# Kernel optimization log

Hardware: AMD Instinct MI355X
Metric: run time of the kernel (lower is better)

## Reference

```python
import jax, jax.numpy as jnp
import numpy as np

N_NODES = 100000
N_EDGES = 3200000
N_GRAPHS = 256
D = 3
H = 32


def _pointnet_layer(h, pos, src, dst, Wa, ba, Wb, bb):
    # PyG convention: edge_index = [src(j), dst(i)]; message uses h_j, pos_j - pos_i
    edge_feat = jnp.concatenate([h[src], pos[src] - pos[dst]], axis=-1)  # [E, Cin+D]
    msg = jax.nn.relu(edge_feat @ Wa + ba) @ Wb + bb                     # [E, H]
    agg = jax.ops.segment_max(msg, dst, num_segments=N_NODES)           # [N, H]
    # PyG scatter-max fills nodes with no incoming edges with 0
    return jnp.where(jnp.isneginf(agg), 0.0, agg)


def setup_inputs() -> dict:
    key = jax.random.key(0)
    ks = jax.random.split(key, 12)
    pos = jax.random.normal(ks[0], (N_NODES, D), dtype=jnp.float32)
    edge_index = jax.random.randint(ks[1], (2, N_EDGES), 0, N_NODES, dtype=jnp.int32)
    batch = jnp.sort(jax.random.randint(ks[2], (N_NODES,), 0, N_GRAPHS, dtype=jnp.int32))
    def lin(k, fan_in, fan_out):
        bound = 1.0 / np.sqrt(fan_in)
        kw, kb = jax.random.split(k)
        W = jax.random.uniform(kw, (fan_in, fan_out), minval=-bound, maxval=bound, dtype=jnp.float32)
        b = jax.random.uniform(kb, (fan_out,), minval=-bound, maxval=bound, dtype=jnp.float32)
        return W, b
    W1a, b1a = lin(ks[3], D + D, H)
    W1b, b1b = lin(ks[4], H, H)
    W2a, b2a = lin(ks[5], H + D, H)
    W2b, b2b = lin(ks[6], H, H)
    Wout, bout = lin(ks[7], H, 1)
    return {"pos": pos, "edge_index": edge_index, "batch": batch,
            "W1a": W1a, "b1a": b1a, "W1b": W1b, "b1b": b1b,
            "W2a": W2a, "b2a": b2a, "W2b": W2b, "b2b": b2b,
            "Wout": Wout, "bout": bout}


def reference(pos, edge_index, batch, W1a, b1a, W1b, b1b, W2a, b2a, W2b, b2b, Wout, bout):
    src, dst = edge_index[0], edge_index[1]
    h = _pointnet_layer(pos, pos, src, dst, W1a, b1a, W1b, b1b)
    h = jax.nn.relu(h)
    h = _pointnet_layer(h, pos, src, dst, W2a, b2a, W2b, b2b)
    h = jax.nn.relu(h)
    g = jax.ops.segment_max(h, batch, num_segments=N_GRAPHS)  # global_max_pool -> [B, H]
    g = jnp.where(jnp.isneginf(g), 0.0, g)
    return g @ Wout + bout  # [B, 1]
```

## Files before the change

### kernel.cpp

```cpp
#include <hip/hip_runtime.h>

#define NN 100000
#define NE 3200000
#define NG 256
#define H 32
#define SB ((NN + 255) / 256)
#define NB 98
#define BK_SH 10
#define PART_BLOCKS ((NE + 4095) / 4096)

typedef __attribute__((ext_vector_type(8))) short b16x8;
typedef __attribute__((ext_vector_type(4))) float f32x4;

union ABfrag { unsigned u[4]; b16x8 v; };

__global__ __launch_bounds__(256) void k_init(unsigned* __restrict__ g,
                                              unsigned* __restrict__ hist,
                                              unsigned* __restrict__ bktcnt) {
    int i = blockIdx.x * 256 + threadIdx.x;
    if (i < NG * H) g[i] = 0u;
    if (i < NN) hist[i] = 0u;
    if (i < NB) bktcnt[i] = 0u;
}

__global__ __launch_bounds__(64) void k_packw(const float* __restrict__ W1b,
                                              const float* __restrict__ W2b,
                                              unsigned* __restrict__ Wpk) {
    int l = threadIdx.x;
    int n = l & 15, gq = l >> 4;
    for (int layer = 0; layer < 2; layer++) {
        const float* W = layer ? W2b : W1b;
        for (int h = 0; h < 2; h++) {
            unsigned hi[8], lo[8];
#pragma unroll
            for (int i = 0; i < 8; i++) {
                float w = W[(8 * gq + i) * H + h * 16 + n];
                unsigned wb = __float_as_uint(w);
                unsigned hb = wb & 0xffff0000u;
                float r = w - __uint_as_float(hb);
                hi[i] = hb;
                lo[i] = __float_as_uint(r) & 0xffff0000u;
            }
            unsigned* dh = Wpk + (((layer * 4 + h * 2 + 0) * 64) + l) * 4;
            unsigned* dl = Wpk + (((layer * 4 + h * 2 + 1) * 64) + l) * 4;
#pragma unroll
            for (int w2 = 0; w2 < 4; w2++) {
                dh[w2] = (hi[2 * w2] >> 16) | (hi[2 * w2 + 1] & 0xffff0000u);
                dl[w2] = (lo[2 * w2] >> 16) | (lo[2 * w2 + 1] & 0xffff0000u);
            }
        }
    }
}

__global__ __launch_bounds__(256) void k_hist(const int* __restrict__ dst,
                                              unsigned* __restrict__ hist,
                                              unsigned* __restrict__ bktcnt) {
    __shared__ unsigned lb[NB];
    int tid = threadIdx.x;
    if (tid < NB) lb[tid] = 0u;
    __syncthreads();
    int base = blockIdx.x * 4096 + tid;
    for (int c = 0; c < 16; c++) {
        int e = base + c * 256;
        if (e < NE) {
            int d = dst[e];
            atomicAdd(&hist[d], 1u);
            atomicAdd(&lb[d >> BK_SH], 1u);
        }
    }
    __syncthreads();
    if (tid < NB) {
        unsigned v = lb[tid];
        if (v) atomicAdd(&bktcnt[tid], v);
    }
}

__global__ __launch_bounds__(256) void k_scan1(const unsigned* __restrict__ hist,
                                               unsigned* __restrict__ pre,
                                               unsigned* __restrict__ bsum) {
    __shared__ unsigned sd[256];
    int tid = threadIdx.x;
    int i = blockIdx.x * 256 + tid;
    unsigned v = (i < NN) ? hist[i] : 0u;
    sd[tid] = v;
    __syncthreads();
    for (int off = 1; off < 256; off <<= 1) {
        unsigned t = (tid >= off) ? sd[tid - off] : 0u;
        __syncthreads();
        sd[tid] += t;
        __syncthreads();
    }
    if (i < NN) pre[i] = sd[tid] - v;
    if (tid == 255) bsum[blockIdx.x] = sd[255];
}

__global__ __launch_bounds__(512) void k_scan2(const unsigned* __restrict__ bsum,
                                               unsigned* __restrict__ bpre) {
    __shared__ unsigned sd[512];
    int t = threadIdx.x;
    unsigned v = (t < SB) ? bsum[t] : 0u;
    sd[t] = v;
    __syncthreads();
    for (int off = 1; off < 512; off <<= 1) {
        unsigned x = (t >= off) ? sd[t - off] : 0u;
        __syncthreads();
        sd[t] += x;
        __syncthreads();
    }
    if (t < SB) bpre[t] = sd[t] - v;
}

__global__ __launch_bounds__(256) void k_scan3(const unsigned* __restrict__ pre,
                                               const unsigned* __restrict__ bpre,
                                               const unsigned* __restrict__ hist,
                                               unsigned* __restrict__ cursors,
                                               unsigned* __restrict__ ends) {
    int i = blockIdx.x * 256 + threadIdx.x;
    if (i < NN) {
        unsigned o = pre[i] + bpre[blockIdx.x];
        cursors[i] = o;
        ends[i] = o + hist[i];
    }
}

__global__ __launch_bounds__(128) void k_bscan(const unsigned* __restrict__ bktcnt,
                                               unsigned* __restrict__ bktbase,
                                               unsigned* __restrict__ bktcur) {
    __shared__ unsigned sd[128];
    int t = threadIdx.x;
    unsigned v = (t < NB) ? bktcnt[t] : 0u;
    sd[t] = v;
    __syncthreads();
    for (int off = 1; off < 128; off <<= 1) {
        unsigned x = (t >= off) ? sd[t - off] : 0u;
        __syncthreads();
        sd[t] += x;
        __syncthreads();
    }
    if (t < NB) { bktbase[t] = sd[t] - v; bktcur[t] = sd[t] - v; }
    if (t == 127) bktbase[NB] = NE;
}

__global__ __launch_bounds__(256) void k_part(const int* __restrict__ src,
                                              const int* __restrict__ dst,
                                              unsigned* __restrict__ bktcur,
                                              unsigned* __restrict__ staging) {
    __shared__ unsigned lh[NB], lcur[NB];
    int tid = threadIdx.x;
    if (tid < NB) lh[tid] = 0u;
    __syncthreads();
    int base = blockIdx.x * 4096 + tid;
    for (int c = 0; c < 16; c++) {
        int e = base + c * 256;
        if (e < NE) atomicAdd(&lh[dst[e] >> BK_SH], 1u);
    }
    __syncthreads();
    if (tid < NB) {
        unsigned v = lh[tid];
        lcur[tid] = v ? atomicAdd(&bktcur[tid], v) : 0u;
    }
    __syncthreads();
    for (int c = 0; c < 16; c++) {
        int e = base + c * 256;
        if (e < NE) {
            int d = dst[e], s = src[e];
            unsigned off = atomicAdd(&lcur[d >> BK_SH], 1u);
            staging[off] = ((unsigned)s << BK_SH) | (unsigned)(d & ((1 << BK_SH) - 1));
        }
    }
}

__global__ __launch_bounds__(256) void k_scat2(const unsigned* __restrict__ staging,
                                               const unsigned* __restrict__ bktbase,
                                               unsigned* __restrict__ cursors,
                                               unsigned* __restrict__ srcS) {
    int i = blockIdx.x * 256 + threadIdx.x;
    unsigned p = staging[i];
    int lo = 0, hi = NB - 1;
    while (lo < hi) {
        int mid = (lo + hi + 1) >> 1;
        if ((unsigned)i >= bktbase[mid]) lo = mid; else hi = mid - 1;
    }
    int d = (lo << BK_SH) | (int)(p & ((1u << BK_SH) - 1));
    unsigned slot = atomicAdd(&cursors[d], 1u);
    srcS[slot] = p >> BK_SH;
}

__global__ __launch_bounds__(256) void k_pre1(const float* __restrict__ pos,
                                              const float* __restrict__ W1a,
                                              const float* __restrict__ b1a,
                                              float* __restrict__ E) {
    int n = blockIdx.x * 256 + threadIdx.x;
    if (n >= NN) return;
    float p0 = pos[3 * n], p1 = pos[3 * n + 1], p2 = pos[3 * n + 2];
    float ev[H];
#pragma unroll
    for (int k = 0; k < H; k++) {
        float v = b1a[k];
        v = fmaf(p0, W1a[k] + W1a[96 + k], v);
        v = fmaf(p1, W1a[32 + k] + W1a[128 + k], v);
        v = fmaf(p2, W1a[64 + k] + W1a[160 + k], v);
        ev[k] = v;
    }
    float4* E4 = (float4*)(E + (size_t)n * H);
#pragma unroll
    for (int r = 0; r < 8; r++)
        E4[r] = make_float4(ev[4 * r], ev[4 * r + 1], ev[4 * r + 2], ev[4 * r + 3]);
}

__global__ __launch_bounds__(256) void k_pre2(const float* __restrict__ pos,
                                              const float* __restrict__ agg,
                                              const float* __restrict__ W2a,
                                              const float* __restrict__ b2a,
                                              float* __restrict__ E) {
    int n = blockIdx.x * 256 + threadIdx.x;
    if (n >= NN) return;
    float h[H];
    const float4* A4 = (const float4*)(agg + (size_t)n * H);
#pragma unroll
    for (int r = 0; r < 8; r++) {
        float4 u = A4[r];
        h[4 * r + 0] = u.x; h[4 * r + 1] = u.y;
        h[4 * r + 2] = u.z; h[4 * r + 3] = u.w;
    }
    float p0 = pos[3 * n], p1 = pos[3 * n + 1], p2 = pos[3 * n + 2];
    float ev[H];
#pragma unroll
    for (int k = 0; k < H; k++) {
        float v = b2a[k];
        v = fmaf(p0, W2a[32 * H + k], v);
        v = fmaf(p1, W2a[33 * H + k], v);
        v = fmaf(p2, W2a[34 * H + k], v);
        ev[k] = v;
    }
#pragma unroll
    for (int j = 0; j < H; j++) {
        float hj = h[j];
#pragma unroll
        for (int k = 0; k < H; k++) ev[k] = fmaf(hj, W2a[j * H + k], ev[k]);
    }
    float4* E4 = (float4*)(E + (size_t)n * H);
#pragma unroll
    for (int r = 0; r < 8; r++)
        E4[r] = make_float4(ev[4 * r], ev[4 * r + 1], ev[4 * r + 2], ev[4 * r + 3]);
}

__global__ __launch_bounds__(256) void k_edge(const unsigned* __restrict__ srcS,
                                              const unsigned* __restrict__ ends,
                                              const float* __restrict__ pos,
                                              const float* __restrict__ E,
                                              const float* __restrict__ Wf,
                                              const unsigned* __restrict__ WpkL,
                                              const float* __restrict__ bb,
                                              float* __restrict__ aggOut,
                                              const int* __restrict__ batch,
                                              unsigned* __restrict__ g,
                                              int layer2) {
    int lane = threadIdx.x & 63;
    int node = __builtin_amdgcn_readfirstlane(blockIdx.x * 4 + (threadIdx.x >> 6));
    unsigned start = (node == 0) ? 0u : ends[node - 1];
    int deg = (int)(ends[node] - start);
    int row = lane & 15;
    int j0 = (lane >> 4) << 3;
    ABfrag b0h, b0l, b1h, b1l;
    {
        const uint4* W4 = (const uint4*)WpkL;
        *(uint4*)b0h.u = W4[0 * 64 + lane];
        *(uint4*)b0l.u = W4[1 * 64 + lane];
        *(uint4*)b1h.u = W4[2 * 64 + lane];
        *(uint4*)b1l.u = W4[3 * 64 + lane];
    }
    float pd0 = pos[3 * node], pd1 = pos[3 * node + 1], pd2 = pos[3 * node + 2];
    float fd[8];
#pragma unroll
    for (int q = 0; q < 8; q++)
        fd[q] = fmaf(pd0, Wf[j0 + q],
                fmaf(pd1, Wf[32 + j0 + q], pd2 * Wf[64 + j0 + q]));
    f32x4 vmax0 = {-3.0e38f, -3.0e38f, -3.0e38f, -3.0e38f};
    f32x4 vmax1 = vmax0;
    const f32x4 z = {0.f, 0.f, 0.f, 0.f};
    for (int i0 = 0; i0 < deg; i0 += 16) {
        int e = i0 + row;
        if (e >= deg) e = deg - 1;
        int s = (int)srcS[start + e];
        const float* er = E + ((size_t)s << 5) + j0;
        float4 t0 = *(const float4*)er;
        float4 t1 = *(const float4*)(er + 4);
        float t[8] = {t0.x, t0.y, t0.z, t0.w, t1.x, t1.y, t1.z, t1.w};
        ABfrag ah, al;
#pragma unroll
        for (int w = 0; w < 4; w++) {
            float x0 = fmaxf(t[2 * w]     - fd[2 * w],     0.f);
            float x1 = fmaxf(t[2 * w + 1] - fd[2 * w + 1], 0.f);
            unsigned u0 = __float_as_uint(x0), u1 = __float_as_uint(x1);
            ah.u[w] = __builtin_amdgcn_perm(u1, u0, 0x07060302u);
            float r0 = x0 - __uint_as_float(u0 & 0xffff0000u);
            float r1 = x1 - __uint_as_float(u1 & 0xffff0000u);
            al.u[w] = __builtin_amdgcn_perm(__float_as_uint(r1),
                                            __float_as_uint(r0), 0x07060302u);
        }
        f32x4 acc0 = __builtin_amdgcn_mfma_f32_16x16x32_bf16(ah.v, b0h.v, z, 0, 0, 0);
        acc0 = __builtin_amdgcn_mfma_f32_16x16x32_bf16(al.v, b0h.v, acc0, 0, 0, 0);
        acc0 = __builtin_amdgcn_mfma_f32_16x16x32_bf16(ah.v, b0l.v, acc0, 0, 0, 0);
        f32x4 acc1 = __builtin_amdgcn_mfma_f32_16x16x32_bf16(ah.v, b1h.v, z, 0, 0, 0);
        acc1 = __builtin_amdgcn_mfma_f32_16x16x32_bf16(al.v, b1h.v, acc1, 0, 0, 0);
        acc1 = __builtin_amdgcn_mfma_f32_16x16x32_bf16(ah.v, b1l.v, acc1, 0, 0, 0);
#pragma unroll
        for (int r = 0; r < 4; r++) {
            vmax0[r] = fmaxf(vmax0[r], acc0[r]);
            vmax1[r] = fmaxf(vmax1[r], acc1[r]);
        }
    }
    float m0 = fmaxf(fmaxf(vmax0[0], vmax0[1]), fmaxf(vmax0[2], vmax0[3]));
    float m1 = fmaxf(fmaxf(vmax1[0], vmax1[1]), fmaxf(vmax1[2], vmax1[3]));
    m0 = fmaxf(m0, __shfl_xor(m0, 16));
    m0 = fmaxf(m0, __shfl_xor(m0, 32));
    m1 = fmaxf(m1, __shfl_xor(m1, 16));
    m1 = fmaxf(m1, __shfl_xor(m1, 32));
    if (lane < H) {
        float red = (lane < 16) ? m0 : m1;
        float val = (deg > 0) ? fmaxf(red + bb[lane], 0.f) : 0.f;
        if (!layer2) {
            aggOut[(size_t)node * H + lane] = val;
        } else {
            int b = batch[node];
            unsigned bits = __float_as_uint(val);
            unsigned* gb = g + ((size_t)b << 5) + lane;
            if (bits > *gb) atomicMax(gb, bits);
        }
    }
}

__global__ __launch_bounds__(256) void k_out(const unsigned* __restrict__ g,
                                             const float* __restrict__ Wout,
                                             const float* __restrict__ bout,
                                             float* __restrict__ out) {
    int bidx = threadIdx.x;
    float acc = bout[0];
#pragma unroll
    for (int k = 0; k < H; k++)
        acc = fmaf(__uint_as_float(g[bidx * H + k]), Wout[k], acc);
    out[bidx] = acc;
}

extern "C" void kernel_launch(void* const* d_in, const int* in_sizes, int n_in,
                              void* d_out, int out_size, void* d_ws, size_t ws_size,
                              hipStream_t stream) {
    const float* pos  = (const float*)d_in[0];
    const int* src    = (const int*)d_in[1];
    const int* dst    = src + NE;
    const int* batch  = (const int*)d_in[2];
    const float* W1a  = (const float*)d_in[3];
    const float* b1a  = (const float*)d_in[4];
    const float* W1b  = (const float*)d_in[5];
    const float* b1b  = (const float*)d_in[6];
    const float* W2a  = (const float*)d_in[7];
    const float* b2a  = (const float*)d_in[8];
    const float* W2b  = (const float*)d_in[9];
    const float* b2b  = (const float*)d_in[10];
    const float* Wout = (const float*)d_in[11];
    const float* bout = (const float*)d_in[12];
    float* out = (float*)d_out;

    const size_t SZ = (size_t)NN * H;
    float*    agg  = (float*)d_ws;
    float*    E    = (float*)d_ws + SZ;
    unsigned* srcS = (unsigned*)d_ws + 2 * SZ;
    unsigned* g    = (unsigned*)d_ws + 3 * SZ;
    unsigned* ends = g + NG * H;
    unsigned* bsum = ends + NN;
    unsigned* bpre = bsum + SB + 1;
    unsigned* Wpk  = bpre + SB + 1;
    unsigned* bktcnt  = Wpk + 4096;
    unsigned* bktbase = bktcnt + NB;
    unsigned* bktcur  = bktbase + NB + 1;
    unsigned* hist    = (unsigned*)agg;
    unsigned* pre     = hist + NN;
    unsigned* cursors = pre + NN;
    unsigned* staging = (unsigned*)E;

    const int NODE_BLOCKS = SB;
    const int SCAT_BLOCKS = NE / 256;
    const int WAVE_BLOCKS = NN / 4;

    k_init<<<NODE_BLOCKS, 256, 0, stream>>>(g, hist, bktcnt);
    k_packw<<<1, 64, 0, stream>>>(W1b, W2b, Wpk);
    k_hist<<<PART_BLOCKS, 256, 0, stream>>>(dst, hist, bktcnt);
    k_scan1<<<NODE_BLOCKS, 256, 0, stream>>>(hist, pre, bsum);
    k_scan2<<<1, 512, 0, stream>>>(bsum, bpre);
    k_scan3<<<NODE_BLOCKS, 256, 0, stream>>>(pre, bpre, hist, cursors, ends);
    k_bscan<<<1, 128, 0, stream>>>(bktcnt, bktbase, bktcur);
    k_part<<<PART_BLOCKS, 256, 0, stream>>>(src, dst, bktcur, staging);
    k_scat2<<<SCAT_BLOCKS, 256, 0, stream>>>(staging, bktbase, cursors, srcS);
    k_pre1<<<NODE_BLOCKS, 256, 0, stream>>>(pos, W1a, b1a, E);
    k_edge<<<WAVE_BLOCKS, 256, 0, stream>>>(srcS, ends, pos, E,
                                            W1a + 3 * H, Wpk, b1b,
                                            agg, batch, g, 0);
    k_pre2<<<NODE_BLOCKS, 256, 0, stream>>>(pos, agg, W2a, b2a, E);
    k_edge<<<WAVE_BLOCKS, 256, 0, stream>>>(srcS, ends, pos, E,
                                            W2a + 32 * H, Wpk + 1024, b2b,
                                            agg, batch, g, 1);
    k_out<<<1, 256, 0, stream>>>(g, Wout, bout, out);
}
```

Before: 656.9 us.

## Split edge gather into four source-range passes for cache locality

Edges are sub-sorted by source window (four ranges of 25000 nodes) within each destination's CSR segment, and each edge kernel runs as four passes. Each pass only gathers E rows from one source window, so the gathered rows (about 3.2MB per window) are meant to stay resident in L2/MALL, and partial maxima are carried through the agg buffer. In exchange it adds extra kernel launches, per-pass read-modify-write of agg, packed 8-bit per-window counts (which overflow if a node has more than 255 in-edges from one window), and a redundant pass over nodes with few edges.

```diff
diff --git a/kernel.cpp b/kernel.cpp
--- a/kernel.cpp
+++ b/kernel.cpp
@@ -8,6 +8,8 @@
 #define NB 98
 #define BK_SH 10
 #define PART_BLOCKS ((NE + 4095) / 4096)
+#define NW 4
+#define WSZ 25000
 
 typedef __attribute__((ext_vector_type(8))) short b16x8;
 typedef __attribute__((ext_vector_type(4))) float f32x4;
@@ -15,11 +17,11 @@
 union ABfrag { unsigned u[4]; b16x8 v; };
 
 __global__ __launch_bounds__(256) void k_init(unsigned* __restrict__ g,
-                                              unsigned* __restrict__ hist,
+                                              uint4* __restrict__ hist2,
                                               unsigned* __restrict__ bktcnt) {
     int i = blockIdx.x * 256 + threadIdx.x;
     if (i < NG * H) g[i] = 0u;
-    if (i < NN) hist[i] = 0u;
+    if (i < NN) hist2[i] = make_uint4(0u, 0u, 0u, 0u);
     if (i < NB) bktcnt[i] = 0u;
 }
 
@@ -52,8 +54,9 @@
     }
 }
 
-__global__ __launch_bounds__(256) void k_hist(const int* __restrict__ dst,
-                                              unsigned* __restrict__ hist,
+__global__ __launch_bounds__(256) void k_hist(const int* __restrict__ src,
+                                              const int* __restrict__ dst,
+                                              unsigned* __restrict__ hist2,
                                               unsigned* __restrict__ bktcnt) {
     __shared__ unsigned lb[NB];
     int tid = threadIdx.x;
@@ -64,7 +67,8 @@
         int e = base + c * 256;
         if (e < NE) {
             int d = dst[e];
-            atomicAdd(&hist[d], 1u);
+            int w = src[e] / WSZ;
+            atomicAdd(&hist2[(d << 2) | w], 1u);
             atomicAdd(&lb[d >> BK_SH], 1u);
         }
     }
@@ -75,13 +79,14 @@
     }
 }
 
-__global__ __launch_bounds__(256) void k_scan1(const unsigned* __restrict__ hist,
+__global__ __launch_bounds__(256) void k_scan1(const uint4* __restrict__ hist2,
                                                unsigned* __restrict__ pre,
                                                unsigned* __restrict__ bsum) {
     __shared__ unsigned sd[256];
     int tid = threadIdx.x;
     int i = blockIdx.x * 256 + tid;
-    unsigned v = (i < NN) ? hist[i] : 0u;
+    unsigned v = 0u;
+    if (i < NN) { uint4 h = hist2[i]; v = h.x + h.y + h.z + h.w; }
     sd[tid] = v;
     __syncthreads();
     for (int off = 1; off < 256; off <<= 1) {
@@ -112,15 +117,28 @@
 
 __global__ __launch_bounds__(256) void k_scan3(const unsigned* __restrict__ pre,
                                                const unsigned* __restrict__ bpre,
-                                               const unsigned* __restrict__ hist,
+                                               const uint4* __restrict__ hist2,
                                                unsigned* __restrict__ cursors,
                                                unsigned* __restrict__ ends) {
     int i = blockIdx.x * 256 + threadIdx.x;
     if (i < NN) {
         unsigned o = pre[i] + bpre[blockIdx.x];
+        uint4 h = hist2[i];
         cursors[i] = o;
-        ends[i] = o + hist[i];
-    }
+        ends[i] = o + h.x + h.y + h.z + h.w;
+    }
+}
+
+__global__ __launch_bounds__(256) void k_cnt(const uint4* __restrict__ hist2,
+                                             const unsigned* __restrict__ cursors,
+                                             uint4* __restrict__ cursors2,
+                                             unsigned* __restrict__ cnt2) {
+    int n = blockIdx.x * 256 + threadIdx.x;
+    if (n >= NN) return;
+    uint4 h = hist2[n];
+    unsigned o = cursors[n];
+    cursors2[n] = make_uint4(o, o + h.x, o + h.x + h.y, o + h.x + h.y + h.z);
+    cnt2[n] = h.x | (h.y << 8) | (h.z << 16) | (h.w << 24);
 }
 
 __global__ __launch_bounds__(128) void k_bscan(const unsigned* __restrict__ bktcnt,
@@ -172,7 +190,7 @@
 
 __global__ __launch_bounds__(256) void k_scat2(const unsigned* __restrict__ staging,
                                                const unsigned* __restrict__ bktbase,
-                                               unsigned* __restrict__ cursors,
+                                               unsigned* __restrict__ cursors2,
                                                unsigned* __restrict__ srcS) {
     int i = blockIdx.x * 256 + threadIdx.x;
     unsigned p = staging[i];
@@ -182,8 +200,10 @@
         if ((unsigned)i >= bktbase[mid]) lo = mid; else hi = mid - 1;
     }
     int d = (lo << BK_SH) | (int)(p & ((1u << BK_SH) - 1));
-    unsigned slot = atomicAdd(&cursors[d], 1u);
-    srcS[slot] = p >> BK_SH;
+    unsigned s = p >> BK_SH;
+    int w = (int)s / WSZ;
+    unsigned slot = atomicAdd(&cursors2[(d << 2) | w], 1u);
+    srcS[slot] = s;
 }
 
 __global__ __launch_bounds__(256) void k_pre1(const float* __restrict__ pos,
@@ -247,6 +267,7 @@
 
 __global__ __launch_bounds__(256) void k_edge(const unsigned* __restrict__ srcS,
                                               const unsigned* __restrict__ ends,
+                                              const unsigned* __restrict__ cnt2,
                                               const float* __restrict__ pos,
                                               const float* __restrict__ E,
                                               const float* __restrict__ Wf,
@@ -255,11 +276,9 @@
                                               float* __restrict__ aggOut,
                                               const int* __restrict__ batch,
                                               unsigned* __restrict__ g,
-                                              int layer2) {
+                                              int layer2, int pass) {
     int lane = threadIdx.x & 63;
-    int node = __builtin_amdgcn_readfirstlane(blockIdx.x * 4 + (threadIdx.x >> 6));
-    unsigned start = (node == 0) ? 0u : ends[node - 1];
-    int deg = (int)(ends[node] - start);
+    int wv = __builtin_amdgcn_readfirstlane(blockIdx.x * 4 + (threadIdx.x >> 6));
     int row = lane & 15;
     int j0 = (lane >> 4) << 3;
     ABfrag b0h, b0l, b1h, b1l;
@@ -270,63 +289,92 @@
         *(uint4*)b1h.u = W4[2 * 64 + lane];
         *(uint4*)b1l.u = W4[3 * 64 + lane];
     }
-    float pd0 = pos[3 * node], pd1 = pos[3 * node + 1], pd2 = pos[3 * node + 2];
-    float fd[8];
-#pragma unroll
-    for (int q = 0; q < 8; q++)
-        fd[q] = fmaf(pd0, Wf[j0 + q],
-                fmaf(pd1, Wf[32 + j0 + q], pd2 * Wf[64 + j0 + q]));
-    f32x4 vmax0 = {-3.0e38f, -3.0e38f, -3.0e38f, -3.0e38f};
-    f32x4 vmax1 = vmax0;
+    float wf0[8], wf1[8], wf2[8];
+#pragma unroll
+    for (int q = 0; q < 8; q++) {
+        wf0[q] = Wf[j0 + q];
+        wf1[q] = Wf[32 + j0 + q];
+        wf2[q] = Wf[64 + j0 + q];
+    }
     const f32x4 z = {0.f, 0.f, 0.f, 0.f};
-    for (int i0 = 0; i0 < deg; i0 += 16) {
-        int e = i0 + row;
-        if (e >= deg) e = deg - 1;
-        int s = (int)srcS[start + e];
-        const float* er = E + ((size_t)s << 5) + j0;
-        float4 t0 = *(const float4*)er;
-        float4 t1 = *(const float4*)(er + 4);
-        float t[8] = {t0.x, t0.y, t0.z, t0.w, t1.x, t1.y, t1.z, t1.w};
-        ABfrag ah, al;
-#pragma unroll
-        for (int w = 0; w < 4; w++) {
-            float x0 = fmaxf(t[2 * w]     - fd[2 * w],     0.f);
-            float x1 = fmaxf(t[2 * w + 1] - fd[2 * w + 1], 0.f);
-            unsigned u0 = __float_as_uint(x0), u1 = __float_as_uint(x1);
-            ah.u[w] = __builtin_amdgcn_perm(u1, u0, 0x07060302u);
-            float r0 = x0 - __uint_as_float(u0 & 0xffff0000u);
-            float r1 = x1 - __uint_as_float(u1 & 0xffff0000u);
-            al.u[w] = __builtin_amdgcn_perm(__float_as_uint(r1),
-                                            __float_as_uint(r0), 0x07060302u);
+    bool fin = (pass == NW - 1);
+#pragma unroll 1
+    for (int nn = 0; nn < 2; nn++) {
+        int node = wv * 2 + nn;
+        unsigned start = (node == 0) ? 0u : ends[node - 1];
+        unsigned c4 = cnt2[node];
+        unsigned c0 = c4 & 255u, c1 = (c4 >> 8) & 255u, c2 = (c4 >> 16) & 255u;
+        unsigned off = start, dw;
+        if (pass == 0)      { dw = c0; }
+        else if (pass == 1) { off += c0; dw = c1; }
+        else if (pass == 2) { off += c0 + c1; dw = c2; }
+        else                { off += c0 + c1 + c2; dw = c4 >> 24; }
+        if (dw == 0u && pass > 0 && !fin) continue;
+        f32x4 vmax0 = {-3.0e38f, -3.0e38f, -3.0e38f, -3.0e38f};
+        f32x4 vmax1 = vmax0;
+        if (dw > 0u) {
+            float pd0 = pos[3 * node], pd1 = pos[3 * node + 1], pd2 = pos[3 * node + 2];
+            float fd[8];
+#pragma unroll
+            for (int q = 0; q < 8; q++)
+                fd[q] = fmaf(pd0, wf0[q], fmaf(pd1, wf1[q], pd2 * wf2[q]));
+            int nt = ((int)dw + 15) >> 4, last = (int)dw - 1;
+            for (int it = 0; it < nt; it++) {
+                int e = (it << 4) + row;
+                if (e > last) e = last;
+                int s = (int)srcS[off + e];
+                const float* er = E + ((size_t)s << 5) + j0;
+                float4 t0 = *(const float4*)er;
+                float4 t1 = *(const float4*)(er + 4);
+                float t[8] = {t0.x, t0.y, t0.z, t0.w, t1.x, t1.y, t1.z, t1.w};
+                ABfrag ah, al;
+#pragma unroll
+                for (int w = 0; w < 4; w++) {
+                    float x0 = fmaxf(t[2 * w]     - fd[2 * w],     0.f);
+                    float x1 = fmaxf(t[2 * w + 1] - fd[2 * w + 1], 0.f);
+                    unsigned u0 = __float_as_uint(x0), u1 = __float_as_uint(x1);
+                    ah.u[w] = __builtin_amdgcn_perm(u1, u0, 0x07060302u);
+                    float r0 = x0 - __uint_as_float(u0 & 0xffff0000u);
+                    float r1 = x1 - __uint_as_float(u1 & 0xffff0000u);
+                    al.u[w] = __builtin_amdgcn_perm(__float_as_uint(r1),
+                                                    __float_as_uint(r0), 0x07060302u);
+                }
+                f32x4 acc0 = __builtin_amdgcn_mfma_f32_16x16x32_bf16(ah.v, b0h.v, z, 0, 0, 0);
+                acc0 = __builtin_amdgcn_mfma_f32_16x16x32_bf16(al.v, b0h.v, acc0, 0, 0, 0);
+                acc0 = __builtin_amdgcn_mfma_f32_16x16x32_bf16(ah.v, b0l.v, acc0, 0, 0, 0);
+                f32x4 acc1 = __builtin_amdgcn_mfma_f32_16x16x32_bf16(ah.v, b1h.v, z, 0, 0, 0);
+                acc1 = __builtin_amdgcn_mfma_f32_16x16x32_bf16(al.v, b1h.v, acc1, 0, 0, 0);
+                acc1 = __builtin_amdgcn_mfma_f32_16x16x32_bf16(ah.v, b1l.v, acc1, 0, 0, 0);
+#pragma unroll
+                for (int r = 0; r < 4; r++) {
+                    vmax0[r] = fmaxf(vmax0[r], acc0[r]);
+                    vmax1[r] = fmaxf(vmax1[r], acc1[r]);
+                }
+            }
         }
-        f32x4 acc0 = __builtin_amdgcn_mfma_f32_16x16x32_bf16(ah.v, b0h.v, z, 0, 0, 0);
-        acc0 = __builtin_amdgcn_mfma_f32_16x16x32_bf16(al.v, b0h.v, acc0, 0, 0, 0);
-        acc0 = __builtin_amdgcn_mfma_f32_16x16x32_bf16(ah.v, b0l.v, acc0, 0, 0, 0);
-        f32x4 acc1 = __builtin_amdgcn_mfma_f32_16x16x32_bf16(ah.v, b1h.v, z, 0, 0, 0);
-        acc1 = __builtin_amdgcn_mfma_f32_16x16x32_bf16(al.v, b1h.v, acc1, 0, 0, 0);
-        acc1 = __builtin_amdgcn_mfma_f32_16x16x32_bf16(ah.v, b1l.v, acc1, 0, 0, 0);
-#pragma unroll
-        for (int r = 0; r < 4; r++) {
-            vmax0[r] = fmaxf(vmax0[r], acc0[r]);
-            vmax1[r] = fmaxf(vmax1[r], acc1[r]);
-        }
-    }
-    float m0 = fmaxf(fmaxf(vmax0[0], vmax0[1]), fmaxf(vmax0[2], vmax0[3]));
-    float m1 = fmaxf(fmaxf(vmax1[0], vmax1[1]), fmaxf(vmax1[2], vmax1[3]));
-    m0 = fmaxf(m0, __shfl_xor(m0, 16));
-    m0 = fmaxf(m0, __shfl_xor(m0, 32));
-    m1 = fmaxf(m1, __shfl_xor(m1, 16));
-    m1 = fmaxf(m1, __shfl_xor(m1, 32));
-    if (lane < H) {
-        float red = (lane < 16) ? m0 : m1;
-        float val = (deg > 0) ? fmaxf(red + bb[lane], 0.f) : 0.f;
-        if (!layer2) {
-            aggOut[(size_t)node * H + lane] = val;
-        } else {
-            int b = batch[node];
-            unsigned bits = __float_as_uint(val);
-            unsigned* gb = g + ((size_t)b << 5) + lane;
-            if (bits > *gb) atomicMax(gb, bits);
+        float m0 = fmaxf(fmaxf(vmax0[0], vmax0[1]), fmaxf(vmax0[2], vmax0[3]));
+        float m1 = fmaxf(fmaxf(vmax1[0], vmax1[1]), fmaxf(vmax1[2], vmax1[3]));
+        m0 = fmaxf(m0, __shfl_xor(m0, 16));
+        m0 = fmaxf(m0, __shfl_xor(m0, 32));
+        m1 = fmaxf(m1, __shfl_xor(m1, 16));
+        m1 = fmaxf(m1, __shfl_xor(m1, 32));
+        if (lane < H) {
+            float red = (lane < 16) ? m0 : m1;
+            float* ar = aggOut + (size_t)node * H;
+            if (pass > 0) red = fmaxf(red, ar[lane]);
+            if (!fin) {
+                ar[lane] = red;
+            } else {
+                float val = fmaxf(red + bb[lane], 0.f);
+                if (!layer2) {
+                    ar[lane] = val;
+                } else {
+                    int b = batch[node];
+                    unsigned bits = __float_as_uint(val);
+                    unsigned* gb = g + ((size_t)b << 5) + lane;
+                    if (bits > *gb) atomicMax(gb, bits);
+                }
+            }
         }
     }
 }
@@ -368,37 +416,43 @@
     unsigned* srcS = (unsigned*)d_ws + 2 * SZ;
     unsigned* g    = (unsigned*)d_ws + 3 * SZ;
     unsigned* ends = g + NG * H;
-    unsigned* bsum = ends + NN;
+    unsigned* cnt2 = ends + NN;
+    unsigned* bsum = cnt2 + NN;
     unsigned* bpre = bsum + SB + 1;
     unsigned* Wpk  = bpre + SB + 1;
     unsigned* bktcnt  = Wpk + 4096;
     unsigned* bktbase = bktcnt + NB;
     unsigned* bktcur  = bktbase + NB + 1;
-    unsigned* hist    = (unsigned*)agg;
-    unsigned* pre     = hist + NN;
-    unsigned* cursors = pre + NN;
-    unsigned* staging = (unsigned*)E;
+    uint4*    hist2    = (uint4*)agg;
+    unsigned* pre      = (unsigned*)agg + 4 * NN;
+    unsigned* cursors  = pre + NN;
+    uint4*    cursors2 = (uint4*)((unsigned*)agg + 6 * NN);
+    unsigned* staging  = (unsigned*)E;
 
     const int NODE_BLOCKS = SB;
     const int SCAT_BLOCKS = NE / 256;
-    const int WAVE_BLOCKS = NN / 4;
-
-    k_init<<<NODE_BLOCKS, 256, 0, stream>>>(g, hist, bktcnt);
+    const int EDGE_BLOCKS = NN / 8;
+
+    k_init<<<NODE_BLOCKS, 256, 0, stream>>>(g, hist2, bktcnt);
     k_packw<<<1, 64, 0, stream>>>(W1b, W2b, Wpk);
-    k_hist<<<PART_BLOCKS, 256, 0, stream>>>(dst, hist, bktcnt);
-    k_scan1<<<NODE_BLOCKS, 256, 0, stream>>>(hist, pre, bsum);
+    k_hist<<<PART_BLOCKS, 256, 0, stream>>>(src, dst, (unsigned*)hist2, bktcnt);
+    k_scan1<<<NODE_BLOCKS, 256, 0, stream>>>(hist2, pre, bsum);
     k_scan2<<<1, 512, 0, stream>>>(bsum, bpre);
-    k_scan3<<<NODE_BLOCKS, 256, 0, stream>>>(pre, bpre, hist, cursors, ends);
+    k_scan3<<<NODE_BLOCKS, 256, 0, stream>>>(pre, bpre, hist2, cursors, ends);
+    k_cnt<<<NODE_BLOCKS, 256, 0, stream>>>(hist2, cursors, cursors2, cnt2);
     k_bscan<<<1, 128, 0, stream>>>(bktcnt, bktbase, bktcur);
     k_part<<<PART_BLOCKS, 256, 0, stream>>>(src, dst, bktcur, staging);
-    k_scat2<<<SCAT_BLOCKS, 256, 0, stream>>>(staging, bktbase, cursors, srcS);
+    k_scat2<<<SCAT_BLOCKS, 256, 0, stream>>>(staging, bktbase,
+                                             (unsigned*)cursors2, srcS);
     k_pre1<<<NODE_BLOCKS, 256, 0, stream>>>(pos, W1a, b1a, E);
-    k_edge<<<WAVE_BLOCKS, 256, 0, stream>>>(srcS, ends, pos, E,
-                                            W1a + 3 * H, Wpk, b1b,
-                                            agg, batch, g, 0);
+    for (int p = 0; p < NW; p++)
+        k_edge<<<EDGE_BLOCKS, 256, 0, stream>>>(srcS, ends, cnt2, pos, E,
+                                                W1a + 3 * H, Wpk, b1b,
+                                                agg, batch, g, 0, p);
     k_pre2<<<NODE_BLOCKS, 256, 0, stream>>>(pos, agg, W2a, b2a, E);
-    k_edge<<<WAVE_BLOCKS, 256, 0, stream>>>(srcS, ends, pos, E,
-                                            W2a + 32 * H, Wpk + 1024, b2b,
-                                            agg, batch, g, 1);
+    for (int p = 0; p < NW; p++)
+        k_edge<<<EDGE_BLOCKS, 256, 0, stream>>>(srcS, ends, cnt2, pos, E,
+                                                W2a + 32 * H, Wpk + 1024, b2b,
+                                                agg, batch, g, 1, p);
     k_out<<<1, 256, 0, stream>>>(g, Wout, bout, out);
 }
```

Result: slower. 843.5 us (+28.4%).
